# Performance work log

Measured on AMD Instinct MI355X. Metric: run time of the kernel, lower is better.

Reference implementation:

```python
import jax, jax.numpy as jnp
from jax import lax
import numpy as np

NPOINT, RADIUS, NSAMPLE = 2048, 0.2, 32
EPS = 1e-5


def fps(xyz, npoint):
    # furthest point sampling; xyz [B,N,3] -> idx [B,npoint] int32
    B, N, _ = xyz.shape

    def body(carry, _):
        dist, far = carry  # dist [B,N], far [B]
        centroid = jnp.take_along_axis(xyz, far[:, None, None], axis=1)  # [B,1,3]
        d = jnp.sum((xyz - centroid) ** 2, -1)  # [B,N]
        dist = jnp.minimum(dist, d)
        nxt = jnp.argmax(dist, -1).astype(jnp.int32)
        return (dist, nxt), far

    init = (jnp.full((B, N), 1e10, xyz.dtype), jnp.zeros((B,), jnp.int32))
    _, idx = lax.scan(body, init, None, length=npoint)
    return jnp.transpose(idx)  # [B, npoint]


def ball_query(radius, nsample, xyz, new_xyz):
    # xyz [B,N,3], new_xyz [B,S,3] -> idx [B,S,nsample] int32
    B, N, _ = xyz.shape
    sqr = jnp.sum((new_xyz[:, :, None, :] - xyz[:, None, :, :]) ** 2, -1)  # [B,S,N]
    idx = jnp.broadcast_to(jnp.arange(N, dtype=jnp.int32), sqr.shape)
    idx = jnp.where(sqr > radius * radius, N, idx)
    idx = jnp.sort(idx, -1)[:, :, :nsample]  # first nsample in-ball indices
    first = idx[:, :, :1]
    return jnp.where(idx == N, first, idx)  # pad misses with first hit


def group(x, idx):
    # x [B,N,C], idx [B,S,K] -> [B,S,K,C]
    return jax.vmap(lambda xb, ib: xb[ib])(x, idx)


def setup_inputs() -> dict:
    key = jax.random.key(0)
    ks = jax.random.split(key, 8)
    B, N = 8, 8192
    mlp, in_c = [32, 32, 64], 6
    inp = {
        'xyz': jax.random.normal(ks[0], (B, N, 3), jnp.float32),
        'points': jax.random.normal(ks[1], (B, N, 3), jnp.float32),
    }
    cin = in_c
    for i, cout in enumerate(mlp):
        inp[f'w{i}'] = jax.random.normal(ks[2 + i], (cout, cin), jnp.float32) * (1.0 / np.sqrt(cin))
        inp[f'b{i}'] = jnp.zeros((cout,), jnp.float32)
        inp[f'g{i}'] = jnp.ones((cout,), jnp.float32)
        inp[f'be{i}'] = jnp.zeros((cout,), jnp.float32)
        cin = cout
    return inp


def reference(xyz, points, w0, b0, g0, be0, w1, b1, g1, be1, w2, b2, g2, be2):
    fps_idx = fps(xyz, NPOINT)
    new_xyz = jax.vmap(lambda xb, ib: xb[ib])(xyz, fps_idx)  # [B,S,3]
    idx = ball_query(RADIUS, NSAMPLE, xyz, new_xyz)  # [B,S,K]
    grouped_xyz = group(xyz, idx) - new_xyz[:, :, None, :]  # [B,S,K,3]
    feat = jnp.concatenate([grouped_xyz, group(points, idx)], -1)  # [B,S,K,6]
    for w, b, g, be in ((w0, b0, g0, be0), (w1, b1, g1, be1), (w2, b2, g2, be2)):
        feat = jnp.einsum('bskc,oc->bsko', feat, w) + b  # 1x1 conv
        mean = jnp.mean(feat, axis=(0, 1, 2))
        var = jnp.var(feat, axis=(0, 1, 2))
        feat = (feat - mean) * lax.rsqrt(var + EPS) * g + be  # BN (train stats)
        feat = jax.nn.relu(feat)
    new_points = jnp.max(feat, axis=2)  # max over neighborhood -> [B,S,64]
    return new_xyz, new_points
```

## Files before the change

### kernel.cpp

```cpp
#include <hip/hip_runtime.h>
#include <math.h>

#define BB 8
#define NN 8192
#define SS 2048
#define KK 32
#define NP (BB*SS*KK)
#define EPSF 1e-5f
#define TT 512

typedef float v2f __attribute__((ext_vector_type(2)));

template <int CTRL>
__device__ __forceinline__ double dpp_max_d(double key) {
    int lo = __double2loint(key), hi = __double2hiint(key);
    int nlo = __builtin_amdgcn_update_dpp(lo, lo, CTRL, 0xf, 0xf, false);
    int nhi = __builtin_amdgcn_update_dpp(hi, hi, CTRL, 0xf, 0xf, false);
    return fmax(__hiloint2double(nhi, nlo), key);
}

__device__ __forceinline__ double wave_max_key(double key) {
    key = dpp_max_d<0x111>(key);
    key = dpp_max_d<0x112>(key);
    key = dpp_max_d<0x114>(key);
    key = dpp_max_d<0x118>(key);
    key = dpp_max_d<0x142>(key);
    key = dpp_max_d<0x143>(key);
    return key;
}

__global__ __launch_bounds__(TT) void fps_kernel(const float* __restrict__ xyz,
                                                 float* __restrict__ out_newxyz) {
#pragma clang fp contract(off)
    const int PPT = NN / TT;
    const int NPAIR = PPT / 2;
    const int NW = TT / 64;
    int b = blockIdx.x;
    int t = threadIdx.x;
    int wid  = t >> 6;
    int lane = t & 63;
    const float* x = xyz + b * NN * 3;
    float* nout = out_newxyz + b * SS * 3;

    __shared__ float4 lxyz[NN];
    __shared__ __align__(16) double skey[2][NW];

    v2f px2[NPAIR], py2[NPAIR], pz2[NPAIR], d2[NPAIR];
    int lo_c[PPT];
#pragma unroll
    for (int s = 0; s < PPT; s++) lo_c[s] = (int)~(unsigned)(t + s * TT);
#pragma unroll
    for (int j = 0; j < NPAIR; j++) {
        int p0 = t + (2 * j) * TT;
        int p1 = p0 + TT;
        float ax = x[p0 * 3 + 0], ay = x[p0 * 3 + 1], az = x[p0 * 3 + 2];
        float bx = x[p1 * 3 + 0], by = x[p1 * 3 + 1], bz = x[p1 * 3 + 2];
        px2[j].x = ax; px2[j].y = bx;
        py2[j].x = ay; py2[j].y = by;
        pz2[j].x = az; pz2[j].y = bz;
        lxyz[p0] = make_float4(ax, ay, az, 0.f);
        lxyz[p1] = make_float4(bx, by, bz, 0.f);
        d2[j].x = 1e10f; d2[j].y = 1e10f;
    }
    __syncthreads();
    float4 c0 = lxyz[0];
    float cx = c0.x, cy = c0.y, cz = c0.z;

#pragma unroll 2
    for (int it = 0; it < SS; it++) {
        float sx = cx, sy = cy, sz = cz;
        if (t == 0) {
            nout[it * 3 + 0] = sx;
            nout[it * 3 + 1] = sy;
            nout[it * 3 + 2] = sz;
        }
        v2f cxx, cyy, czz;
        cxx.x = cx; cxx.y = cx;
        cyy.x = cy; cyy.y = cy;
        czz.x = cz; czz.y = cz;
        double acc[4] = {0.0, 0.0, 0.0, 0.0};
#pragma unroll
        for (int j = 0; j < NPAIR; j++) {
            v2f dx = px2[j] - cxx;
            v2f dy = py2[j] - cyy;
            v2f dz = pz2[j] - czz;
            v2f ss = (dx * dx + dy * dy) + dz * dz;
            v2f e  = __builtin_elementwise_min(d2[j], ss);
            d2[j] = e;
            double k0 = __hiloint2double(__float_as_int(e.x), lo_c[2 * j]);
            double k1 = __hiloint2double(__float_as_int(e.y), lo_c[2 * j + 1]);
            double kp = fmax(k0, k1);
            acc[j & 3] = fmax(acc[j & 3], kp);
        }
        double key = fmax(fmax(acc[0], acc[1]), fmax(acc[2], acc[3]));
        key = wave_max_key(key);
        if (lane == 63) skey[it & 1][wid] = key;
        __syncthreads();
        const double2* sk = (const double2*)&skey[it & 1][0];
        double2 k01 = sk[0];
        double2 k23 = sk[1];
        double2 k45 = sk[2];
        double2 k67 = sk[3];
        double ka = fmax(fmax(k01.x, k01.y), fmax(k23.x, k23.y));
        double kb = fmax(fmax(k45.x, k45.y), fmax(k67.x, k67.y));
        double k  = fmax(ka, kb);
        int gi = (int)(~(unsigned)__double2loint(k)) & (NN - 1);
        float4 c = lxyz[gi];
        cx = c.x; cy = c.y; cz = c.z;
    }
}

__global__ __launch_bounds__(256) void ballq_kernel(const float* __restrict__ xyz,
                                                    const float* __restrict__ new_xyz,
                                                    int* __restrict__ idx_out) {
    int q    = blockIdx.x * 4 + (threadIdx.x >> 6);
    int lane = threadIdx.x & 63;
    int b    = q >> 11;
    const float* x = xyz + b * NN * 3;
    const float* c = new_xyz + q * 3;
    float cx = c[0], cy = c[1], cz = c[2];
    int* out = idx_out + q * KK;
    const float R2 = (float)(0.2 * 0.2);

    int count = 0;
    int first = -1;
    for (int base = 0; base < NN; base += 64) {
        int p = base + lane;
        float dx = __fsub_rn(x[p * 3 + 0], cx);
        float dy = __fsub_rn(x[p * 3 + 1], cy);
        float dz = __fsub_rn(x[p * 3 + 2], cz);
        float d  = __fadd_rn(__fadd_rn(__fmul_rn(dx, dx), __fmul_rn(dy, dy)),
                             __fmul_rn(dz, dz));
        bool in = !(d > R2);
        unsigned long long m = __ballot(in);
        if (first < 0 && m != 0ull) first = base + __ffsll((unsigned long long)m) - 1;
        int pre = __popcll(m & ((1ull << lane) - 1ull));
        int pos = count + pre;
        if (in && pos < KK) out[pos] = p;
        count += __popcll(m);
        if (count >= KK) break;
    }
    for (int i2 = count + lane; i2 < KK; i2 += 64) out[i2] = first;
}

__device__ __forceinline__ void load_in6(const float* __restrict__ xyz,
                                         const float* __restrict__ points,
                                         const float* __restrict__ new_xyz,
                                         const int* __restrict__ idx, int p, float inx[6]) {
    int bs = p >> 5;
    int b  = bs >> 11;
    int pt = idx[p];
    const float* xb = xyz + ((long)b * NN + pt) * 3;
    const float* pb = points + ((long)b * NN + pt) * 3;
    const float* nx = new_xyz + bs * 3;
    inx[0] = xb[0] - nx[0];
    inx[1] = xb[1] - nx[1];
    inx[2] = xb[2] - nx[2];
    inx[3] = pb[0];
    inx[4] = pb[1];
    inx[5] = pb[2];
}

template <int CIN, int COUT>
__device__ __forceinline__ void linear(const float* __restrict__ w,
                                       const float* __restrict__ bias,
                                       const float* xin, float* yout) {
#pragma unroll
    for (int o = 0; o < COUT; o++) {
        float acc = bias[o];
#pragma unroll
        for (int j = 0; j < CIN; j++) acc = fmaf(w[o * CIN + j], xin[j], acc);
        yout[o] = acc;
    }
}

template <int C>
__device__ __forceinline__ void bn_coef(const float* __restrict__ stats,
                                        const float* __restrict__ g,
                                        const float* __restrict__ be,
                                        float* s_sc, float* s_sh) {
    int t = threadIdx.x;
    if (t < C) {
        float mean = stats[t] * (1.0f / (float)NP);
        float var  = stats[C + t] * (1.0f / (float)NP) - mean * mean;
        float rstd = 1.0f / sqrtf(var + EPSF);
        float sc = g[t] * rstd;
        s_sc[t] = sc;
        s_sh[t] = be[t] - mean * sc;
    }
    __syncthreads();
}

template <int C>
__device__ __forceinline__ void accum_stats(const float* y, float* __restrict__ gstats) {
    __shared__ float buf[256][33];
    int t = threadIdx.x;
#pragma unroll
    for (int h = 0; h < C / 32; h++) {
        __syncthreads();
#pragma unroll
        for (int c = 0; c < 32; c++) buf[t][c] = y[h * 32 + c];
        __syncthreads();
        if (t < 32) {
            float s = 0.f, sq = 0.f;
            for (int r = 0; r < 256; r++) {
                float v = buf[r][t];
                s += v;
                sq = fmaf(v, v, sq);
            }
            atomicAdd(&gstats[h * 32 + t], s);
            atomicAdd(&gstats[C + h * 32 + t], sq);
        }
    }
}

__global__ __launch_bounds__(256) void l0_stats_kernel(
    const float* __restrict__ xyz, const float* __restrict__ points,
    const float* __restrict__ new_xyz, const int* __restrict__ idx,
    const float* __restrict__ w0, const float* __restrict__ b0_,
    float* __restrict__ stats0) {
    int p = blockIdx.x * 256 + threadIdx.x;
    float inx[6];
    load_in6(xyz, points, new_xyz, idx, p, inx);
    float y0[32];
    linear<6, 32>(w0, b0_, inx, y0);
    accum_stats<32>(y0, stats0);
}

__global__ __launch_bounds__(256) void l1_stats_kernel(
    const float* __restrict__ xyz, const float* __restrict__ points,
    const float* __restrict__ new_xyz, const int* __restrict__ idx,
    const float* __restrict__ w0, const float* __restrict__ b0_,
    const float* __restrict__ g0, const float* __restrict__ be0,
    const float* __restrict__ w1, const float* __restrict__ b1_,
    const float* __restrict__ stats0, float* __restrict__ stats1) {
    __shared__ float sc0[32], sh0[32];
    bn_coef<32>(stats0, g0, be0, sc0, sh0);
    int p = blockIdx.x * 256 + threadIdx.x;
    float inx[6];
    load_in6(xyz, points, new_xyz, idx, p, inx);
    float y0[32];
    linear<6, 32>(w0, b0_, inx, y0);
#pragma unroll
    for (int c = 0; c < 32; c++) y0[c] = fmaxf(fmaf(y0[c], sc0[c], sh0[c]), 0.f);
    float y1[32];
    linear<32, 32>(w1, b1_, y0, y1);
    accum_stats<32>(y1, stats1);
}

__global__ __launch_bounds__(256) void l2_stats_kernel(
    const float* __restrict__ xyz, const float* __restrict__ points,
    const float* __restrict__ new_xyz, const int* __restrict__ idx,
    const float* __restrict__ w0, const float* __restrict__ b0_,
    const float* __restrict__ g0, const float* __restrict__ be0,
    const float* __restrict__ w1, const float* __restrict__ b1_,
    const float* __restrict__ g1, const float* __restrict__ be1,
    const float* __restrict__ w2, const float* __restrict__ b2_,
    const float* __restrict__ stats0, const float* __restrict__ stats1,
    float* __restrict__ stats2) {
    __shared__ float sc0[32], sh0[32], sc1[32], sh1[32];
    bn_coef<32>(stats0, g0, be0, sc0, sh0);
    bn_coef<32>(stats1, g1, be1, sc1, sh1);
    int p = blockIdx.x * 256 + threadIdx.x;
    float inx[6];
    load_in6(xyz, points, new_xyz, idx, p, inx);
    float y0[32];
    linear<6, 32>(w0, b0_, inx, y0);
#pragma unroll
    for (int c = 0; c < 32; c++) y0[c] = fmaxf(fmaf(y0[c], sc0[c], sh0[c]), 0.f);
    float y1[32];
    linear<32, 32>(w1, b1_, y0, y1);
#pragma unroll
    for (int c = 0; c < 32; c++) y1[c] = fmaxf(fmaf(y1[c], sc1[c], sh1[c]), 0.f);
    float y2[64];
    linear<32, 64>(w2, b2_, y1, y2);
    accum_stats<64>(y2, stats2);
}

__global__ __launch_bounds__(256) void final_kernel(
    const float* __restrict__ xyz, const float* __restrict__ points,
    const float* __restrict__ new_xyz, const int* __restrict__ idx,
    const float* __restrict__ w0, const float* __restrict__ b0_,
    const float* __restrict__ g0, const float* __restrict__ be0,
    const float* __restrict__ w1, const float* __restrict__ b1_,
    const float* __restrict__ g1, const float* __restrict__ be1,
    const float* __restrict__ w2, const float* __restrict__ b2_,
    const float* __restrict__ g2, const float* __restrict__ be2,
    const float* __restrict__ stats0, const float* __restrict__ stats1,
    const float* __restrict__ stats2, float* __restrict__ out_points) {
    __shared__ float sc0[32], sh0[32], sc1[32], sh1[32], sc2[64], sh2[64];
    bn_coef<32>(stats0, g0, be0, sc0, sh0);
    bn_coef<32>(stats1, g1, be1, sc1, sh1);
    bn_coef<64>(stats2, g2, be2, sc2, sh2);
    int p = blockIdx.x * 256 + threadIdx.x;
    float inx[6];
    load_in6(xyz, points, new_xyz, idx, p, inx);
    float y0[32];
    linear<6, 32>(w0, b0_, inx, y0);
#pragma unroll
    for (int c = 0; c < 32; c++) y0[c] = fmaxf(fmaf(y0[c], sc0[c], sh0[c]), 0.f);
    float y1[32];
    linear<32, 32>(w1, b1_, y0, y1);
#pragma unroll
    for (int c = 0; c < 32; c++) y1[c] = fmaxf(fmaf(y1[c], sc1[c], sh1[c]), 0.f);
    float y2[64];
    linear<32, 64>(w2, b2_, y1, y2);
#pragma unroll
    for (int c = 0; c < 64; c++) {
        float v = fmaxf(fmaf(y2[c], sc2[c], sh2[c]), 0.f);
#pragma unroll
        for (int off = 1; off < 32; off <<= 1)
            v = fmaxf(v, __shfl_xor(v, off));
        y2[c] = v;
    }
    int lane = threadIdx.x & 63;
    if ((lane & 31) == 0) {
        int bs = p >> 5;
        float4* o = (float4*)(out_points + (long)bs * 64);
#pragma unroll
        for (int c4 = 0; c4 < 16; c4++)
            o[c4] = make_float4(y2[c4 * 4], y2[c4 * 4 + 1], y2[c4 * 4 + 2], y2[c4 * 4 + 3]);
    }
}

extern "C" void kernel_launch(void* const* d_in, const int* in_sizes, int n_in,
                              void* d_out, int out_size, void* d_ws, size_t ws_size,
                              hipStream_t stream) {
    (void)in_sizes; (void)n_in; (void)out_size; (void)ws_size;
    const float* xyz    = (const float*)d_in[0];
    const float* points = (const float*)d_in[1];
    const float* w0  = (const float*)d_in[2];
    const float* b0_ = (const float*)d_in[3];
    const float* g0  = (const float*)d_in[4];
    const float* be0 = (const float*)d_in[5];
    const float* w1  = (const float*)d_in[6];
    const float* b1_ = (const float*)d_in[7];
    const float* g1  = (const float*)d_in[8];
    const float* be1 = (const float*)d_in[9];
    const float* w2  = (const float*)d_in[10];
    const float* b2_ = (const float*)d_in[11];
    const float* g2  = (const float*)d_in[12];
    const float* be2 = (const float*)d_in[13];

    float* out        = (float*)d_out;
    float* out_newxyz = out;
    float* out_points = out + BB * SS * 3;

    int*   idx    = (int*)d_ws;
    float* stats  = (float*)d_ws + NP;
    float* stats0 = stats;
    float* stats1 = stats + 64;
    float* stats2 = stats + 128;

    hipMemsetAsync(stats, 0, 256 * sizeof(float), stream);

    fps_kernel<<<BB, TT, 0, stream>>>(xyz, out_newxyz);
    ballq_kernel<<<BB * SS / 4, 256, 0, stream>>>(xyz, out_newxyz, idx);
    l0_stats_kernel<<<NP / 256, 256, 0, stream>>>(xyz, points, out_newxyz, idx, w0, b0_, stats0);
    l1_stats_kernel<<<NP / 256, 256, 0, stream>>>(xyz, points, out_newxyz, idx,
                                                  w0, b0_, g0, be0, w1, b1_, stats0, stats1);
    l2_stats_kernel<<<NP / 256, 256, 0, stream>>>(xyz, points, out_newxyz, idx,
                                                  w0, b0_, g0, be0, w1, b1_, g1, be1,
                                                  w2, b2_, stats0, stats1, stats2);
    final_kernel<<<NP / 256, 256, 0, stream>>>(xyz, points, out_newxyz, idx,
                                               w0, b0_, g0, be0, w1, b1_, g1, be1,
                                               w2, b2_, g2, be2, stats0, stats1, stats2,
                                               out_points);
}
```

Measured before the change: 2.033 ms.

## Use LDS atomicMax for FPS argmax and fuse layer-0 stats into ball query

FPS now reduces each wave's packed distance/index key with a 64-bit LDS atomicMax into a triple-buffered slot, instead of writing per-wave keys and doing a post-barrier 8-way max. This shortens the serial critical path after each barrier, at the cost of LDS atomic latency before it. The layer-0 BN statistics pass is merged into the ball-query kernel, which removes one launch and a pass over idx; half of each block's threads feed zeros into the stats reduction.

```diff
diff --git a/kernel.cpp b/kernel.cpp
--- a/kernel.cpp
+++ b/kernel.cpp
@@ -34,16 +34,14 @@
 #pragma clang fp contract(off)
     const int PPT = NN / TT;
     const int NPAIR = PPT / 2;
-    const int NW = TT / 64;
     int b = blockIdx.x;
     int t = threadIdx.x;
-    int wid  = t >> 6;
     int lane = t & 63;
     const float* x = xyz + b * NN * 3;
     float* nout = out_newxyz + b * SS * 3;
 
     __shared__ float4 lxyz[NN];
-    __shared__ __align__(16) double skey[2][NW];
+    __shared__ __align__(16) unsigned long long skey3[3];
 
     v2f px2[NPAIR], py2[NPAIR], pz2[NPAIR], d2[NPAIR];
     int lo_c[PPT];
@@ -62,10 +60,12 @@
         lxyz[p1] = make_float4(bx, by, bz, 0.f);
         d2[j].x = 1e10f; d2[j].y = 1e10f;
     }
+    if (t == 0) { skey3[0] = 0ull; skey3[1] = 0ull; skey3[2] = 0ull; }
     __syncthreads();
     float4 c0 = lxyz[0];
     float cx = c0.x, cy = c0.y, cz = c0.z;
 
+    int sl = 0;
 #pragma unroll 2
     for (int it = 0; it < SS; it++) {
         float sx = cx, sy = cy, sz = cz;
@@ -73,6 +73,7 @@
             nout[it * 3 + 0] = sx;
             nout[it * 3 + 1] = sy;
             nout[it * 3 + 2] = sz;
+            skey3[sl == 2 ? 0 : sl + 1] = 0ull;
         }
         v2f cxx, cyy, czz;
         cxx.x = cx; cxx.y = cx;
@@ -94,25 +95,95 @@
         }
         double key = fmax(fmax(acc[0], acc[1]), fmax(acc[2], acc[3]));
         key = wave_max_key(key);
-        if (lane == 63) skey[it & 1][wid] = key;
+        if (lane == 63)
+            atomicMax(&skey3[sl], (unsigned long long)__double_as_longlong(key));
         __syncthreads();
-        const double2* sk = (const double2*)&skey[it & 1][0];
-        double2 k01 = sk[0];
-        double2 k23 = sk[1];
-        double2 k45 = sk[2];
-        double2 k67 = sk[3];
-        double ka = fmax(fmax(k01.x, k01.y), fmax(k23.x, k23.y));
-        double kb = fmax(fmax(k45.x, k45.y), fmax(k67.x, k67.y));
-        double k  = fmax(ka, kb);
-        int gi = (int)(~(unsigned)__double2loint(k)) & (NN - 1);
+        unsigned long long k = skey3[sl];
+        int gi = (int)(~(unsigned)k) & (NN - 1);
         float4 c = lxyz[gi];
         cx = c.x; cy = c.y; cz = c.z;
+        sl = (sl == 2) ? 0 : sl + 1;
+    }
+}
+
+__device__ __forceinline__ void load_in6(const float* __restrict__ xyz,
+                                         const float* __restrict__ points,
+                                         const float* __restrict__ new_xyz,
+                                         const int* __restrict__ idx, int p, float inx[6]) {
+    int bs = p >> 5;
+    int b  = bs >> 11;
+    int pt = idx[p];
+    const float* xb = xyz + ((long)b * NN + pt) * 3;
+    const float* pb = points + ((long)b * NN + pt) * 3;
+    const float* nx = new_xyz + bs * 3;
+    inx[0] = xb[0] - nx[0];
+    inx[1] = xb[1] - nx[1];
+    inx[2] = xb[2] - nx[2];
+    inx[3] = pb[0];
+    inx[4] = pb[1];
+    inx[5] = pb[2];
+}
+
+template <int CIN, int COUT>
+__device__ __forceinline__ void linear(const float* __restrict__ w,
+                                       const float* __restrict__ bias,
+                                       const float* xin, float* yout) {
+#pragma unroll
+    for (int o = 0; o < COUT; o++) {
+        float acc = bias[o];
+#pragma unroll
+        for (int j = 0; j < CIN; j++) acc = fmaf(w[o * CIN + j], xin[j], acc);
+        yout[o] = acc;
+    }
+}
+
+template <int C>
+__device__ __forceinline__ void bn_coef(const float* __restrict__ stats,
+                                        const float* __restrict__ g,
+                                        const float* __restrict__ be,
+                                        float* s_sc, float* s_sh) {
+    int t = threadIdx.x;
+    if (t < C) {
+        float mean = stats[t] * (1.0f / (float)NP);
+        float var  = stats[C + t] * (1.0f / (float)NP) - mean * mean;
+        float rstd = 1.0f / sqrtf(var + EPSF);
+        float sc = g[t] * rstd;
+        s_sc[t] = sc;
+        s_sh[t] = be[t] - mean * sc;
+    }
+    __syncthreads();
+}
+
+template <int C>
+__device__ __forceinline__ void accum_stats(const float* y, float* __restrict__ gstats) {
+    __shared__ float buf[256][33];
+    int t = threadIdx.x;
+#pragma unroll
+    for (int h = 0; h < C / 32; h++) {
+        __syncthreads();
+#pragma unroll
+        for (int c = 0; c < 32; c++) buf[t][c] = y[h * 32 + c];
+        __syncthreads();
+        if (t < 32) {
+            float s = 0.f, sq = 0.f;
+            for (int r = 0; r < 256; r++) {
+                float v = buf[r][t];
+                s += v;
+                sq = fmaf(v, v, sq);
+            }
+            atomicAdd(&gstats[h * 32 + t], s);
+            atomicAdd(&gstats[C + h * 32 + t], sq);
+        }
     }
 }
 
 __global__ __launch_bounds__(256) void ballq_kernel(const float* __restrict__ xyz,
                                                     const float* __restrict__ new_xyz,
-                                                    int* __restrict__ idx_out) {
+                                                    int* __restrict__ idx_out,
+                                                    const float* __restrict__ points,
+                                                    const float* __restrict__ w0,
+                                                    const float* __restrict__ b0_,
+                                                    float* __restrict__ stats0) {
     int q    = blockIdx.x * 4 + (threadIdx.x >> 6);
     int lane = threadIdx.x & 63;
     int b    = q >> 11;
@@ -141,90 +212,20 @@
         if (count >= KK) break;
     }
     for (int i2 = count + lane; i2 < KK; i2 += 64) out[i2] = first;
-}
-
-__device__ __forceinline__ void load_in6(const float* __restrict__ xyz,
-                                         const float* __restrict__ points,
-                                         const float* __restrict__ new_xyz,
-                                         const int* __restrict__ idx, int p, float inx[6]) {
-    int bs = p >> 5;
-    int b  = bs >> 11;
-    int pt = idx[p];
-    const float* xb = xyz + ((long)b * NN + pt) * 3;
-    const float* pb = points + ((long)b * NN + pt) * 3;
-    const float* nx = new_xyz + bs * 3;
-    inx[0] = xb[0] - nx[0];
-    inx[1] = xb[1] - nx[1];
-    inx[2] = xb[2] - nx[2];
-    inx[3] = pb[0];
-    inx[4] = pb[1];
-    inx[5] = pb[2];
-}
-
-template <int CIN, int COUT>
-__device__ __forceinline__ void linear(const float* __restrict__ w,
-                                       const float* __restrict__ bias,
-                                       const float* xin, float* yout) {
-#pragma unroll
-    for (int o = 0; o < COUT; o++) {
-        float acc = bias[o];
-#pragma unroll
-        for (int j = 0; j < CIN; j++) acc = fmaf(w[o * CIN + j], xin[j], acc);
-        yout[o] = acc;
-    }
-}
-
-template <int C>
-__device__ __forceinline__ void bn_coef(const float* __restrict__ stats,
-                                        const float* __restrict__ g,
-                                        const float* __restrict__ be,
-                                        float* s_sc, float* s_sh) {
+
+    __syncthreads();
     int t = threadIdx.x;
-    if (t < C) {
-        float mean = stats[t] * (1.0f / (float)NP);
-        float var  = stats[C + t] * (1.0f / (float)NP) - mean * mean;
-        float rstd = 1.0f / sqrtf(var + EPSF);
-        float sc = g[t] * rstd;
-        s_sc[t] = sc;
-        s_sh[t] = be[t] - mean * sc;
-    }
-    __syncthreads();
-}
-
-template <int C>
-__device__ __forceinline__ void accum_stats(const float* y, float* __restrict__ gstats) {
-    __shared__ float buf[256][33];
-    int t = threadIdx.x;
-#pragma unroll
-    for (int h = 0; h < C / 32; h++) {
-        __syncthreads();
-#pragma unroll
-        for (int c = 0; c < 32; c++) buf[t][c] = y[h * 32 + c];
-        __syncthreads();
-        if (t < 32) {
-            float s = 0.f, sq = 0.f;
-            for (int r = 0; r < 256; r++) {
-                float v = buf[r][t];
-                s += v;
-                sq = fmaf(v, v, sq);
-            }
-            atomicAdd(&gstats[h * 32 + t], s);
-            atomicAdd(&gstats[C + h * 32 + t], sq);
-        }
-    }
-}
-
-__global__ __launch_bounds__(256) void l0_stats_kernel(
-    const float* __restrict__ xyz, const float* __restrict__ points,
-    const float* __restrict__ new_xyz, const int* __restrict__ idx,
-    const float* __restrict__ w0, const float* __restrict__ b0_,
-    float* __restrict__ stats0) {
-    int p = blockIdx.x * 256 + threadIdx.x;
-    float inx[6];
-    load_in6(xyz, points, new_xyz, idx, p, inx);
-    float y0[32];
-    linear<6, 32>(w0, b0_, inx, y0);
-    accum_stats<32>(y0, stats0);
+    float y0s[32];
+    if (t < 128) {
+        int p = blockIdx.x * 128 + t;
+        float inx[6];
+        load_in6(xyz, points, new_xyz, idx_out, p, inx);
+        linear<6, 32>(w0, b0_, inx, y0s);
+    } else {
+#pragma unroll
+        for (int cc = 0; cc < 32; cc++) y0s[cc] = 0.f;
+    }
+    accum_stats<32>(y0s, stats0);
 }
 
 __global__ __launch_bounds__(256) void l1_stats_kernel(
@@ -355,8 +356,8 @@
     hipMemsetAsync(stats, 0, 256 * sizeof(float), stream);
 
     fps_kernel<<<BB, TT, 0, stream>>>(xyz, out_newxyz);
-    ballq_kernel<<<BB * SS / 4, 256, 0, stream>>>(xyz, out_newxyz, idx);
-    l0_stats_kernel<<<NP / 256, 256, 0, stream>>>(xyz, points, out_newxyz, idx, w0, b0_, stats0);
+    ballq_kernel<<<BB * SS / 4, 256, 0, stream>>>(xyz, out_newxyz, idx,
+                                                  points, w0, b0_, stats0);
     l1_stats_kernel<<<NP / 256, 256, 0, stream>>>(xyz, points, out_newxyz, idx,
                                                   w0, b0_, g0, be0, w1, b1_, stats0, stats1);
     l2_stats_kernel<<<NP / 256, 256, 0, stream>>>(xyz, points, out_newxyz, idx,
```

New measurement: 2.218 ms. 9.1% more time.
